# Kernel tuning notes

Hardware: AMD Instinct MI355X
Metric: run time of the kernel (lower is better)

The kernel has to match this reference:

```python
import jax, jax.numpy as jnp
import numpy as np

N_LAYERS = 2
D_CONV = 4
D_MODEL = 768
D_INNER = 1536
D_STATE = 16
D_DELTA = 48
B = 2
L = 1024
EPS = 1e-5


def setup_inputs() -> dict:
    key = jax.random.key(0)
    ks = jax.random.split(key, 8)
    s = 0.02
    x = jax.random.normal(ks[0], (B, L, D_MODEL), jnp.float32)
    in_proj_w = jax.random.normal(ks[1], (N_LAYERS, 2 * D_INNER, D_MODEL), jnp.float32) * s
    conv_w = jax.random.normal(ks[2], (N_LAYERS, D_INNER, 1, D_CONV), jnp.float32) * s
    conv_b = jnp.zeros((N_LAYERS, D_INNER), jnp.float32)
    xproj_w = jax.random.normal(ks[3], (N_LAYERS, D_DELTA + 2 * D_STATE, D_INNER), jnp.float32) * s
    dt_w = jax.random.normal(ks[4], (N_LAYERS, D_INNER, D_DELTA), jnp.float32) * s
    dt_b = jax.random.normal(ks[5], (N_LAYERS, D_INNER), jnp.float32) * s
    A_log = jnp.tile(jnp.log(jnp.arange(1, D_STATE + 1, dtype=jnp.float32)), (N_LAYERS, D_INNER, 1))
    D = jnp.ones((N_LAYERS, D_INNER), jnp.float32)
    out_proj_w = jax.random.normal(ks[6], (N_LAYERS, D_MODEL, D_INNER), jnp.float32) * s
    norm_w = jnp.ones((N_LAYERS, D_MODEL), jnp.float32)
    return dict(x=x, in_proj_w=in_proj_w, conv_w=conv_w, conv_b=conv_b,
                xproj_w=xproj_w, dt_w=dt_w, dt_b=dt_b, A_log=A_log, D=D,
                out_proj_w=out_proj_w, norm_w=norm_w)


def rms_norm(x, w):
    return w * x * jax.lax.rsqrt(jnp.mean(x * x, axis=-1, keepdims=True) + EPS)


def causal_depthwise_conv(x, w, b):
    # x: [B, L, D_INNER], w: [D_INNER, 1, K], b: [D_INNER]
    xc = x.transpose(0, 2, 1)  # [B, D, L]
    y = jax.lax.conv_general_dilated(
        xc, w, window_strides=(1,), padding=[(D_CONV - 1, 0)],
        dimension_numbers=("NCH", "OIH", "NCH"), feature_group_count=D_INNER)
    y = y + b[None, :, None]
    return y.transpose(0, 2, 1)  # [B, L, D]


def ssm(x, A_log, D, xproj_w, dt_w, dt_b):
    # x: [B, L, D_INNER]
    A = -jnp.exp(A_log)  # [D, N]
    dbc = jnp.einsum('bld,ed->ble', x, xproj_w)
    delta, Bc, C = jnp.split(dbc, [D_DELTA, D_DELTA + D_STATE], axis=-1)
    delta = jax.nn.softplus(jnp.einsum('blr,dr->bld', delta, dt_w) + dt_b)  # [B, L, D]
    dA = jnp.exp(delta[..., None] * A)                          # [B, L, D, N]
    dBx = delta[..., None] * Bc[:, :, None, :] * x[..., None]   # [B, L, D, N]

    def step(h, inp):
        dA_t, dBx_t, C_t = inp
        h = dA_t * h + dBx_t                      # [B, D, N]
        y = jnp.einsum('bdn,bn->bd', h, C_t)      # [B, D]
        return h, y

    h0 = jnp.zeros((x.shape[0], D_INNER, D_STATE), x.dtype)
    _, ys = jax.lax.scan(step, h0, (dA.transpose(1, 0, 2, 3),
                                    dBx.transpose(1, 0, 2, 3),
                                    C.transpose(1, 0, 2)))
    y = ys.transpose(1, 0, 2)  # [B, L, D]
    return y + D * x


def mamba_block(x, in_w, cw, cb, xp_w, dtw, dtb, Alog, Dp, out_w):
    xz = jnp.einsum('blm,em->ble', x, in_w)           # [B, L, 2*D_INNER]
    xi, z = jnp.split(xz, 2, axis=-1)
    xi = jax.nn.silu(causal_depthwise_conv(xi, cw, cb))
    y = ssm(xi, Alog, Dp, xp_w, dtw, dtb)
    out = y * jax.nn.silu(z)
    return jnp.einsum('bld,md->blm', out, out_w)


def reference(x, in_proj_w, conv_w, conv_b, xproj_w, dt_w, dt_b, A_log, D, out_proj_w, norm_w):
    for i in range(N_LAYERS):
        x = x + mamba_block(rms_norm(x, norm_w[i]), in_proj_w[i], conv_w[i], conv_b[i],
                            xproj_w[i], dt_w[i], dt_b[i], A_log[i], D[i], out_proj_w[i])
    return x
```

## Files before the change

kernel.cpp:

```cpp
#include <hip/hip_runtime.h>
#include <hip/hip_bf16.h>
#include <cstdint>

#define NL 2
#define DM 768
#define DI 1536
#define DS 16
#define DD 48
#define DCONV 4
#define BB 2
#define LL 1024
#define MROWS (BB*LL)
#define DBCW (DD + 2*DS)
#define TC 16
#define NCH (LL/TC)
#define KSPL 4
#define XPN 128

typedef __bf16 bf16x8 __attribute__((ext_vector_type(8)));
typedef float f32x4 __attribute__((ext_vector_type(4)));
using bf16 = __hip_bfloat16;

__device__ __forceinline__ float softplusf(float x) {
  return (x > 20.f) ? x : log1pf(__expf(x));
}

__device__ __forceinline__ float bfu2f(ushort u) {
  return __uint_as_float((uint32_t)u << 16);
}

__device__ __forceinline__ void load_lds16(const void* g, void* l) {
  __builtin_amdgcn_global_load_lds(
      (const __attribute__((address_space(1))) void*)g,
      (__attribute__((address_space(3))) void*)l, 16, 0, 0);
}

#define WI_N (NL*2*DI*DM)
#define WX_N (NL*XPN*DI)
#define WD_N (NL*DI*DD)
#define WO_N (NL*DM*DI)
__global__ __launch_bounds__(256)
void prep_weights(const float* __restrict__ wi, const float* __restrict__ wx,
                  const float* __restrict__ wd, const float* __restrict__ wo,
                  bf16* __restrict__ bi, bf16* __restrict__ bx,
                  bf16* __restrict__ bd, bf16* __restrict__ bo)
{
  int i = blockIdx.x * 256 + threadIdx.x;
  if (i < WI_N) { bi[i] = __float2bfloat16(wi[i]); return; }
  i -= WI_N;
  if (i < WX_N) {
    const int l = i / (XPN*DI), r = (i / DI) % XPN, k = i % DI;
    const float v = (r < DBCW) ? wx[((size_t)l*DBCW + r)*DI + k] : 0.f;
    bx[i] = __float2bfloat16(v); return;
  }
  i -= WX_N;
  if (i < WD_N) { bd[i] = __float2bfloat16(wd[i]); return; }
  i -= WD_N;
  if (i < WO_N) { bo[i] = __float2bfloat16(wo[i]); }
}

__global__ __launch_bounds__(256)
void rmsnorm_kernel(const float* __restrict__ x, const float* __restrict__ w,
                    bf16* __restrict__ out)
{
  const int row = blockIdx.x;
  const float* xr = x + (size_t)row * DM;
  const int t = threadIdx.x;
  float v0 = xr[t], v1 = xr[t + 256], v2 = xr[t + 512];
  float ss = v0*v0 + v1*v1 + v2*v2;
  #pragma unroll
  for (int off = 32; off > 0; off >>= 1) ss += __shfl_down(ss, off);
  __shared__ float sred[4];
  if ((t & 63) == 0) sred[t >> 6] = ss;
  __syncthreads();
  const float scale = rsqrtf((sred[0]+sred[1]+sred[2]+sred[3]) * (1.f/DM) + 1e-5f);
  out[(size_t)row*DM + t      ] = __float2bfloat16(v0 * scale * w[t]);
  out[(size_t)row*DM + t + 256] = __float2bfloat16(v1 * scale * w[t + 256]);
  out[(size_t)row*DM + t + 512] = __float2bfloat16(v2 * scale * w[t + 512]);
}

__global__ __launch_bounds__(256)
void gemm_in128(const bf16* __restrict__ A, const bf16* __restrict__ W,
                bf16* __restrict__ xb, bf16* __restrict__ zb)
{
  __shared__ __align__(16) bf16 As[128][32];
  __shared__ __align__(16) bf16 Ws[128][32];
  const int tid = threadIdx.x;
  const int wave = tid >> 6, lane = tid & 63;
  const int m0 = blockIdx.x * 128, n0 = blockIdx.y * 128;
  const int wr = (wave >> 1) * 64, wc = (wave & 1) * 64;
  const int l16 = lane & 15, quad = lane >> 4;
  const int srow = wave * 16 + (lane >> 2);
  const int scol = (lane & 3) * 8;
  bf16* a_base0 = &As[wave*16][0];
  bf16* a_base1 = &As[64 + wave*16][0];
  bf16* w_base0 = &Ws[wave*16][0];
  bf16* w_base1 = &Ws[64 + wave*16][0];

  f32x4 acc[4][4] = {};

  for (int k0 = 0; k0 < DM; k0 += 32) {
    load_lds16(A + (size_t)(m0 + srow) * DM + k0 + scol,      a_base0);
    load_lds16(A + (size_t)(m0 + 64 + srow) * DM + k0 + scol, a_base1);
    load_lds16(W + (size_t)(n0 + srow) * DM + k0 + scol,      w_base0);
    load_lds16(W + (size_t)(n0 + 64 + srow) * DM + k0 + scol, w_base1);
    __syncthreads();

    bf16x8 af[4], wf[4];
    #pragma unroll
    for (int i = 0; i < 4; ++i)
      af[i] = *reinterpret_cast<const bf16x8*>(&As[wr + i*16 + l16][quad*8]);
    #pragma unroll
    for (int j = 0; j < 4; ++j)
      wf[j] = *reinterpret_cast<const bf16x8*>(&Ws[wc + j*16 + l16][quad*8]);
    #pragma unroll
    for (int i = 0; i < 4; ++i)
      #pragma unroll
      for (int j = 0; j < 4; ++j)
        acc[i][j] = __builtin_amdgcn_mfma_f32_16x16x32_bf16(af[i], wf[j], acc[i][j], 0, 0, 0);
    __syncthreads();
  }

  const bool isz = (n0 >= DI);
  #pragma unroll
  for (int i = 0; i < 4; ++i) {
    #pragma unroll
    for (int j = 0; j < 4; ++j) {
      const int col = n0 + wc + j*16 + l16;
      #pragma unroll
      for (int r = 0; r < 4; ++r) {
        const int row = m0 + wr + i*16 + quad*4 + r;
        const float v = acc[i][j][r];
        if (!isz) xb[(size_t)row*DI + col]      = __float2bfloat16(v);
        else      zb[(size_t)row*DI + col - DI] = __float2bfloat16(v);
      }
    }
  }
}

template<int MODE>
__global__ __launch_bounds__(256)
void gemm64l(const bf16* __restrict__ A, int lda,
             const bf16* __restrict__ W, int ldw,
             float* __restrict__ C, int ldc, int N, int K,
             const float* __restrict__ res)
{
  __shared__ __align__(16) bf16 As[64][32];
  __shared__ __align__(16) bf16 Ws[64][32];
  const int tid = threadIdx.x;
  const int wave = tid >> 6, lane = tid & 63;
  const int m0 = blockIdx.x * 64, n0 = blockIdx.y * 64;
  const int wr = (wave >> 1) * 32, wc = (wave & 1) * 32;
  const int l16 = lane & 15, quad = lane >> 4;
  const int srow = wave * 16 + (lane >> 2);
  const int scol = (lane & 3) * 8;
  bf16* a_base = &As[wave*16][0];
  bf16* w_base = &Ws[wave*16][0];

  A += (size_t)blockIdx.z * K;
  W += (size_t)blockIdx.z * K;
  C += (size_t)blockIdx.z * MROWS * ldc;

  f32x4 acc[2][2] = {};

  for (int k0 = 0; k0 < K; k0 += 32) {
    load_lds16(A + (size_t)(m0 + srow) * lda + k0 + scol, a_base);
    load_lds16(W + (size_t)(n0 + srow) * ldw + k0 + scol, w_base);
    __syncthreads();
    bf16x8 af[2], wf[2];
    #pragma unroll
    for (int i = 0; i < 2; ++i)
      af[i] = *reinterpret_cast<const bf16x8*>(&As[wr + i*16 + l16][quad*8]);
    #pragma unroll
    for (int j = 0; j < 2; ++j)
      wf[j] = *reinterpret_cast<const bf16x8*>(&Ws[wc + j*16 + l16][quad*8]);
    #pragma unroll
    for (int i = 0; i < 2; ++i)
      #pragma unroll
      for (int j = 0; j < 2; ++j)
        acc[i][j] = __builtin_amdgcn_mfma_f32_16x16x32_bf16(af[i], wf[j], acc[i][j], 0, 0, 0);
    __syncthreads();
  }

  #pragma unroll
  for (int i = 0; i < 2; ++i) {
    #pragma unroll
    for (int j = 0; j < 2; ++j) {
      const int col = n0 + wc + j*16 + l16;
      if (col >= N) continue;
      #pragma unroll
      for (int r = 0; r < 4; ++r) {
        const int row = m0 + wr + i*16 + quad*4 + r;
        float v = acc[i][j][r];
        const size_t idx = (size_t)row * ldc + col;
        if (MODE == 3) v += res[idx];
        C[idx] = v;
      }
    }
  }
}

__global__ __launch_bounds__(256)
void xproj_reduce(const float* __restrict__ part, bf16* __restrict__ dbcb,
                  float* __restrict__ bcf)
{
  const int idx = blockIdx.x * 256 + threadIdx.x;
  const int row = idx / DBCW, col = idx % DBCW;
  float v = part[idx];
  #pragma unroll
  for (int z = 1; z < KSPL; ++z) v += part[idx + (size_t)z*MROWS*DBCW];
  if (col < DD) dbcb[(size_t)row*DD + col] = __float2bfloat16(v);
  else          bcf[(size_t)row*32 + col - DD] = v;
}

__global__ __launch_bounds__(256)
void conv_silu_kernel(const bf16* __restrict__ xb, const float* __restrict__ cw,
                      const float* __restrict__ cb, bf16* __restrict__ xob)
{
  const int idx = blockIdx.x * 256 + threadIdx.x;
  const int d = idx % DI;
  const int row = idx / DI;
  const int l = row % LL;
  float acc = cb[d];
  #pragma unroll
  for (int k = 0; k < DCONV; ++k) {
    const int ll = l - (DCONV-1) + k;
    if (ll >= 0)
      acc += cw[d*DCONV + k] * __bfloat162float(xb[(size_t)(row - (DCONV-1) + k) * DI + d]);
  }
  const float s = acc / (1.f + __expf(-acc));
  xob[idx] = __float2bfloat16(s);
}

__global__ __launch_bounds__(256)
void gemm_dt(const bf16* __restrict__ A, const bf16* __restrict__ W,
             bf16* __restrict__ Cb, const float* __restrict__ bias)
{
  __shared__ __align__(16) bf16 As[64][40];
  __shared__ __align__(16) bf16 Ws[64][40];
  const int tid = threadIdx.x;
  const int m0 = blockIdx.x * 64, n0 = blockIdx.y * 64;
  const int wave = tid >> 6, lane = tid & 63;
  const int wr = (wave >> 1) * 32, wc = (wave & 1) * 32;
  const int l16 = lane & 15, quad = lane >> 4;
  const int srow = tid >> 2;
  const int scol = (tid & 3) * 8;

  f32x4 acc[2][2] = {};

  #pragma unroll
  for (int k0 = 0; k0 < DD; k0 += 32) {
    {
      const bf16* src = A + (size_t)(m0 + srow) * DD + (k0 + scol);
      bf16* dst = &As[srow][scol];
      if (k0 + scol + 8 <= DD) {
        *reinterpret_cast<uint4*>(dst) = *reinterpret_cast<const uint4*>(src);
      } else {
        #pragma unroll
        for (int j = 0; j < 8; ++j)
          dst[j] = (k0 + scol + j < DD) ? src[j] : __float2bfloat16(0.f);
      }
    }
    {
      const bf16* src = W + (size_t)(n0 + srow) * DD + (k0 + scol);
      bf16* dst = &Ws[srow][scol];
      if (k0 + scol + 8 <= DD) {
        *reinterpret_cast<uint4*>(dst) = *reinterpret_cast<const uint4*>(src);
      } else {
        #pragma unroll
        for (int j = 0; j < 8; ++j)
          dst[j] = (k0 + scol + j < DD) ? src[j] : __float2bfloat16(0.f);
      }
    }
    __syncthreads();
    bf16x8 af[2], wf[2];
    #pragma unroll
    for (int i = 0; i < 2; ++i)
      af[i] = *reinterpret_cast<const bf16x8*>(&As[wr + i*16 + l16][quad*8]);
    #pragma unroll
    for (int j = 0; j < 2; ++j)
      wf[j] = *reinterpret_cast<const bf16x8*>(&Ws[wc + j*16 + l16][quad*8]);
    #pragma unroll
    for (int i = 0; i < 2; ++i)
      #pragma unroll
      for (int j = 0; j < 2; ++j)
        acc[i][j] = __builtin_amdgcn_mfma_f32_16x16x32_bf16(af[i], wf[j], acc[i][j], 0, 0, 0);
    __syncthreads();
  }

  #pragma unroll
  for (int i = 0; i < 2; ++i) {
    #pragma unroll
    for (int j = 0; j < 2; ++j) {
      const int col = n0 + wc + j*16 + l16;
      #pragma unroll
      for (int r = 0; r < 4; ++r) {
        const int row = m0 + wr + i*16 + quad*4 + r;
        Cb[(size_t)row*DI + col] = __float2bfloat16(softplusf(acc[i][j][r] + bias[col]));
      }
    }
  }
}

__global__ __launch_bounds__(256)
void scan_pass1(const bf16* __restrict__ delta, const bf16* __restrict__ xi,
                const float* __restrict__ bcf, const float* __restrict__ A_log,
                float* __restrict__ P, float* __restrict__ H)
{
  __shared__ float Bs[TC][DS];
  const int tid = threadIdx.x;
  const int wave = tid >> 6, lane = tid & 63;
  const int s = lane >> 5;
  const int dloc = wave*32 + (lane & 31);
  const int dt = blockIdx.x % (DI/128);
  const int c  = (blockIdx.x / (DI/128)) % NCH;
  const int b  =  blockIdx.x / ((DI/128)*NCH);
  const int d  = dt*128 + dloc;
  const int t0 = c*TC;

  {
    const int t = tid >> 4, n = tid & 15;
    Bs[t][n] = bcf[((size_t)b*LL + t0 + t)*32 + n];
  }

  const ushort* dptr = (const ushort*)(delta + ((size_t)b*LL + t0)*DI + d);
  const ushort* xptr = (const ushort*)(xi    + ((size_t)b*LL + t0)*DI + d);
  ushort dls[TC], xvs[TC];
  #pragma unroll
  for (int t = 0; t < TC; ++t) dls[t] = dptr[(size_t)t*DI];
  #pragma unroll
  for (int t = 0; t < TC; ++t) xvs[t] = xptr[(size_t)t*DI];

  float An[8];
  {
    const float4* ap = (const float4*)(A_log + (size_t)d*DS + s*8);
    float4 v0 = ap[0], v1 = ap[1];
    An[0] = -__expf(v0.x)*1.44269504f; An[1] = -__expf(v0.y)*1.44269504f;
    An[2] = -__expf(v0.z)*1.44269504f; An[3] = -__expf(v0.w)*1.44269504f;
    An[4] = -__expf(v1.x)*1.44269504f; An[5] = -__expf(v1.y)*1.44269504f;
    An[6] = -__expf(v1.z)*1.44269504f; An[7] = -__expf(v1.w)*1.44269504f;
  }
  __syncthreads();

  float h[8] = {0.f,0.f,0.f,0.f,0.f,0.f,0.f,0.f};
  float sdl = 0.f;
  #pragma unroll
  for (int t = 0; t < TC; ++t) {
    const float dl = bfu2f(dls[t]);
    const float xv = bfu2f(xvs[t]);
    const float dlxv = dl * xv;
    sdl += dl;
    const float4* brow = (const float4*)&Bs[t][s*8];
    const float4 b0 = brow[0], b1 = brow[1];
    const float bb[8] = {b0.x,b0.y,b0.z,b0.w,b1.x,b1.y,b1.z,b1.w};
    #pragma unroll
    for (int n = 0; n < 8; ++n) {
      const float dA = exp2f(dl * An[n]);
      h[n] = dA*h[n] + dlxv*bb[n];
    }
  }
  const size_t base = (((size_t)b*NCH + c)*DI + d)*DS + s*8;
  float4* Pp = (float4*)(P + base);
  float4* Hp = (float4*)(H + base);
  Pp[0] = make_float4(exp2f(An[0]*sdl), exp2f(An[1]*sdl), exp2f(An[2]*sdl), exp2f(An[3]*sdl));
  Pp[1] = make_float4(exp2f(An[4]*sdl), exp2f(An[5]*sdl), exp2f(An[6]*sdl), exp2f(An[7]*sdl));
  Hp[0] = make_float4(h[0],h[1],h[2],h[3]);
  Hp[1] = make_float4(h[4],h[5],h[6],h[7]);
}

__global__ __launch_bounds__(256)
void scan_fix(const float* __restrict__ P, float* __restrict__ H)
{
  const int idx = blockIdx.x * 256 + threadIdx.x;
  const int n = idx & 15;
  const int d = (idx >> 4) % DI;
  const int b = idx / (DS * DI);
  float hin = 0.f;
  #pragma unroll 8
  for (int c = 0; c < NCH; ++c) {
    const size_t ic = (((size_t)b*NCH + c)*DI + d)*DS + n;
    const float Pv = P[ic];
    const float Hv = H[ic];
    H[ic] = hin;
    hin = fmaf(Pv, hin, Hv);
  }
}

__global__ __launch_bounds__(256)
void scan_pass2(const bf16* __restrict__ delta, const bf16* __restrict__ xi,
                const float* __restrict__ bcf, const float* __restrict__ A_log,
                const float* __restrict__ H, const float* __restrict__ Dp,
                const bf16* __restrict__ zb, bf16* __restrict__ outb)
{
  __shared__ float Bs[TC][DS];
  __shared__ float Cs[TC][DS];
  const int tid = threadIdx.x;
  const int wave = tid >> 6, lane = tid & 63;
  const int s = lane >> 5;
  const int dloc = wave*32 + (lane & 31);
  const int dt = blockIdx.x % (DI/128);
  const int c  = (blockIdx.x / (DI/128)) % NCH;
  const int b  =  blockIdx.x / ((DI/128)*NCH);
  const int d  = dt*128 + dloc;
  const int t0 = c*TC;

  {
    const int t = tid >> 4, n = tid & 15;
    const size_t r0 = ((size_t)b*LL + t0 + t)*32;
    Bs[t][n] = bcf[r0 + n];
    Cs[t][n] = bcf[r0 + 16 + n];
  }

  const ushort* dptr = (const ushort*)(delta + ((size_t)b*LL + t0)*DI + d);
  const ushort* xptr = (const ushort*)(xi    + ((size_t)b*LL + t0)*DI + d);
  const ushort* zptr = (const ushort*)(zb    + ((size_t)b*LL + t0)*DI + d);
  ushort dls[TC], xvs[TC], zvs[TC];
  #pragma unroll
  for (int t = 0; t < TC; ++t) dls[t] = dptr[(size_t)t*DI];
  #pragma unroll
  for (int t = 0; t < TC; ++t) xvs[t] = xptr[(size_t)t*DI];
  #pragma unroll
  for (int t = 0; t < TC; ++t) zvs[t] = zptr[(size_t)t*DI];

  float An[8];
  {
    const float4* ap = (const float4*)(A_log + (size_t)d*DS + s*8);
    float4 v0 = ap[0], v1 = ap[1];
    An[0] = -__expf(v0.x)*1.44269504f; An[1] = -__expf(v0.y)*1.44269504f;
    An[2] = -__expf(v0.z)*1.44269504f; An[3] = -__expf(v0.w)*1.44269504f;
    An[4] = -__expf(v1.x)*1.44269504f; An[5] = -__expf(v1.y)*1.44269504f;
    An[6] = -__expf(v1.z)*1.44269504f; An[7] = -__expf(v1.w)*1.44269504f;
  }
  const float Dd = Dp[d];
  float h[8];
  {
    const float4* hp = (const float4*)(H + (((size_t)b*NCH + c)*DI + d)*DS + s*8);
    float4 h0 = hp[0], h1 = hp[1];
    h[0]=h0.x; h[1]=h0.y; h[2]=h0.z; h[3]=h0.w;
    h[4]=h1.x; h[5]=h1.y; h[6]=h1.z; h[7]=h1.w;
  }
  __syncthreads();

  bf16* optr = outb + ((size_t)b*LL + t0)*DI + d;

  #pragma unroll
  for (int t = 0; t < TC; ++t) {
    const float dl = bfu2f(dls[t]);
    const float xv = bfu2f(xvs[t]);
    const float zv = bfu2f(zvs[t]);
    const float dlxv = dl * xv;
    const float4* brow = (const float4*)&Bs[t][s*8];
    const float4* crow = (const float4*)&Cs[t][s*8];
    const float4 b0 = brow[0], b1 = brow[1];
    const float4 c0 = crow[0], c1 = crow[1];
    const float bb[8] = {b0.x,b0.y,b0.z,b0.w,b1.x,b1.y,b1.z,b1.w};
    const float cc[8] = {c0.x,c0.y,c0.z,c0.w,c1.x,c1.y,c1.z,c1.w};
    float y = 0.f;
    #pragma unroll
    for (int n = 0; n < 8; ++n) {
      const float dA = exp2f(dl * An[n]);
      h[n] = dA*h[n] + dlxv*bb[n];
      y = fmaf(h[n], cc[n], y);
    }
    y += __shfl_xor(y, 32);
    if (s == 0) {
      const float o = (y + Dd * xv) * (zv / (1.f + __expf(-zv)));
      optr[(size_t)t*DI] = __float2bfloat16(o);
    }
  }
}

extern "C" void kernel_launch(void* const* d_in, const int* in_sizes, int n_in,
                              void* d_out, int out_size, void* d_ws, size_t ws_size,
                              hipStream_t stream)
{
  const float* x_in   = (const float*)d_in[0];
  const float* w_inp  = (const float*)d_in[1];
  const float* w_conv = (const float*)d_in[2];
  const float* b_conv = (const float*)d_in[3];
  const float* w_xprj = (const float*)d_in[4];
  const float* w_dtp  = (const float*)d_in[5];
  const float* b_dt   = (const float*)d_in[6];
  const float* a_log  = (const float*)d_in[7];
  const float* d_par  = (const float*)d_in[8];
  const float* w_outp = (const float*)d_in[9];
  const float* w_norm = (const float*)d_in[10];
  float* xfinal = (float*)d_out;

  char* ws = (char*)d_ws;
  size_t off = 0;
  auto alloc = [&](size_t bytes) -> void* {
    void* p = ws + off;
    off += (bytes + 255) & ~(size_t)255;
    return p;
  };
  bf16*  wb_in  = (bf16*) alloc((size_t)WI_N*2);
  bf16*  wb_xp  = (bf16*) alloc((size_t)WX_N*2);
  bf16*  wb_dt  = (bf16*) alloc((size_t)WD_N*2);
  bf16*  wb_out = (bf16*) alloc((size_t)WO_N*2);
  bf16*  xn     = (bf16*) alloc((size_t)MROWS*DM*2);
  bf16*  xb     = (bf16*) alloc((size_t)MROWS*DI*2);
  bf16*  zb     = (bf16*) alloc((size_t)MROWS*DI*2);
  bf16*  xcb    = (bf16*) alloc((size_t)MROWS*DI*2);
  float* xpart  = (float*)alloc((size_t)KSPL*MROWS*DBCW*4);
  bf16*  dbcb   = (bf16*) alloc((size_t)MROWS*DD*2);
  float* bcf    = (float*)alloc((size_t)MROWS*32*4);
  bf16*  dltb   = (bf16*) alloc((size_t)MROWS*DI*2);
  bf16*  scb    = (bf16*) alloc((size_t)MROWS*DI*2);
  float* x1     = (float*)alloc((size_t)MROWS*DM*4);
  float* Pws    = (float*)alloc((size_t)BB*NCH*DI*DS*4);
  float* Hws    = (float*)alloc((size_t)BB*NCH*DI*DS*4);

  prep_weights<<<(WI_N+WX_N+WD_N+WO_N + 255)/256, 256, 0, stream>>>(
      w_inp, w_xprj, w_dtp, w_outp, wb_in, wb_xp, wb_dt, wb_out);

  const float* xprev = x_in;
  for (int l = 0; l < NL; ++l) {
    rmsnorm_kernel<<<MROWS, 256, 0, stream>>>(xprev, w_norm + l*DM, xn);

    gemm_in128<<<dim3(MROWS/128, (2*DI)/128), 256, 0, stream>>>(
        xn, wb_in + (size_t)l*2*DI*DM, xb, zb);

    conv_silu_kernel<<<(MROWS*DI)/256, 256, 0, stream>>>(
        xb, w_conv + l*DI*DCONV, b_conv + l*DI, xcb);

    gemm64l<0><<<dim3(MROWS/64, XPN/64, KSPL), 256, 0, stream>>>(
        xcb, DI, wb_xp + (size_t)l*XPN*DI, DI, xpart, DBCW, DBCW, DI/KSPL, nullptr);

    xproj_reduce<<<(MROWS*DBCW)/256, 256, 0, stream>>>(xpart, dbcb, bcf);

    gemm_dt<<<dim3(MROWS/64, DI/64), 256, 0, stream>>>(
        dbcb, wb_dt + (size_t)l*DI*DD, dltb, b_dt + l*DI);

    scan_pass1<<<BB*NCH*(DI/128), 256, 0, stream>>>(
        dltb, xcb, bcf, a_log + (size_t)l*DI*DS, Pws, Hws);
    scan_fix<<<(BB*DI*DS)/256, 256, 0, stream>>>(Pws, Hws);
    scan_pass2<<<BB*NCH*(DI/128), 256, 0, stream>>>(
        dltb, xcb, bcf, a_log + (size_t)l*DI*DS, Hws, d_par + l*DI, zb, scb);

    float* xout = (l == NL-1) ? xfinal : x1;
    gemm64l<3><<<dim3(MROWS/64, DM/64, 1), 256, 0, stream>>>(
        scb, DI, wb_out + (size_t)l*DM*DI, DI, xout, DM, DM, DI, xprev);

    xprev = x1;
  }
}
```

Baseline: 364.5 us.

## Fuse x-proj split-K reduce into consumers, vectorize conv, shrink scan carry state

Removes the xproj_reduce kernel: gemm_dt now sums the split-K partials for delta directly while staging its A tile, and both scan passes sum the B/C partials into shared memory themselves. Conv+SiLU processes 8 channels per thread with vector loads and stores. Scan pass1 writes only the per-chunk delta sum instead of full P decay tensors, and scan_fix recomputes the decay with exp2. Scan chunk length doubles to 32. This cuts launches and intermediate traffic at the cost of redundant partial reductions and higher register pressure in the scan kernels.

Result: no change. 364.5 us (+0.0%).

```diff
diff --git a/kernel.cpp b/kernel.cpp
--- a/kernel.cpp
+++ b/kernel.cpp
@@ -12,13 +12,14 @@
 #define LL 1024
 #define MROWS (BB*LL)
 #define DBCW (DD + 2*DS)
-#define TC 16
+#define TC 32
 #define NCH (LL/TC)
 #define KSPL 4
 #define XPN 128
 
 typedef __bf16 bf16x8 __attribute__((ext_vector_type(8)));
 typedef float f32x4 __attribute__((ext_vector_type(4)));
+typedef ushort ushort8 __attribute__((ext_vector_type(8)));
 using bf16 = __hip_bfloat16;
 
 __device__ __forceinline__ float softplusf(float x) {
@@ -27,6 +28,11 @@
 
 __device__ __forceinline__ float bfu2f(ushort u) {
   return __uint_as_float((uint32_t)u << 16);
+}
+
+__device__ __forceinline__ ushort f2bfu(float f) {
+  const bf16 h = __float2bfloat16(f);
+  return *reinterpret_cast<const ushort*>(&h);
 }
 
 __device__ __forceinline__ void load_lds16(const void* g, void* l) {
@@ -201,39 +207,51 @@
 }
 
 __global__ __launch_bounds__(256)
-void xproj_reduce(const float* __restrict__ part, bf16* __restrict__ dbcb,
-                  float* __restrict__ bcf)
-{
-  const int idx = blockIdx.x * 256 + threadIdx.x;
-  const int row = idx / DBCW, col = idx % DBCW;
-  float v = part[idx];
-  #pragma unroll
-  for (int z = 1; z < KSPL; ++z) v += part[idx + (size_t)z*MROWS*DBCW];
-  if (col < DD) dbcb[(size_t)row*DD + col] = __float2bfloat16(v);
-  else          bcf[(size_t)row*32 + col - DD] = v;
-}
-
-__global__ __launch_bounds__(256)
 void conv_silu_kernel(const bf16* __restrict__ xb, const float* __restrict__ cw,
                       const float* __restrict__ cb, bf16* __restrict__ xob)
 {
   const int idx = blockIdx.x * 256 + threadIdx.x;
-  const int d = idx % DI;
-  const int row = idx / DI;
+  const int d8 = idx % (DI/8);
+  const int row = idx / (DI/8);
   const int l = row % LL;
-  float acc = cb[d];
+  const int d0 = d8 * 8;
+
+  float4 cwv[8];
+  #pragma unroll
+  for (int j = 0; j < 8; ++j)
+    cwv[j] = reinterpret_cast<const float4*>(cw)[d0 + j];
+
+  float acc[8];
+  {
+    const float4* cbp = reinterpret_cast<const float4*>(cb + d0);
+    float4 c0 = cbp[0], c1 = cbp[1];
+    acc[0]=c0.x; acc[1]=c0.y; acc[2]=c0.z; acc[3]=c0.w;
+    acc[4]=c1.x; acc[5]=c1.y; acc[6]=c1.z; acc[7]=c1.w;
+  }
   #pragma unroll
   for (int k = 0; k < DCONV; ++k) {
     const int ll = l - (DCONV-1) + k;
-    if (ll >= 0)
-      acc += cw[d*DCONV + k] * __bfloat162float(xb[(size_t)(row - (DCONV-1) + k) * DI + d]);
-  }
-  const float s = acc / (1.f + __expf(-acc));
-  xob[idx] = __float2bfloat16(s);
-}
-
-__global__ __launch_bounds__(256)
-void gemm_dt(const bf16* __restrict__ A, const bf16* __restrict__ W,
+    if (ll >= 0) {
+      const ushort8 v = *reinterpret_cast<const ushort8*>(
+          xb + (size_t)(row - (DCONV-1) + k) * DI + d0);
+      #pragma unroll
+      for (int j = 0; j < 8; ++j) {
+        const float w = (k==0) ? cwv[j].x : (k==1) ? cwv[j].y : (k==2) ? cwv[j].z : cwv[j].w;
+        acc[j] += w * bfu2f(v[j]);
+      }
+    }
+  }
+  ushort8 o;
+  #pragma unroll
+  for (int j = 0; j < 8; ++j) {
+    const float s = acc[j] / (1.f + __expf(-acc[j]));
+    o[j] = f2bfu(s);
+  }
+  *reinterpret_cast<ushort8*>(xob + (size_t)row*DI + d0) = o;
+}
+
+__global__ __launch_bounds__(256)
+void gemm_dt(const float* __restrict__ xpart, const bf16* __restrict__ W,
              bf16* __restrict__ Cb, const float* __restrict__ bias)
 {
   __shared__ __align__(16) bf16 As[64][40];
@@ -251,14 +269,22 @@
   #pragma unroll
   for (int k0 = 0; k0 < DD; k0 += 32) {
     {
-      const bf16* src = A + (size_t)(m0 + srow) * DD + (k0 + scol);
+      const int cbase = k0 + scol;
       bf16* dst = &As[srow][scol];
-      if (k0 + scol + 8 <= DD) {
-        *reinterpret_cast<uint4*>(dst) = *reinterpret_cast<const uint4*>(src);
+      if (cbase < DD) {
+        float a[8] = {0,0,0,0,0,0,0,0};
+        #pragma unroll
+        for (int z = 0; z < KSPL; ++z) {
+          const float4* p = reinterpret_cast<const float4*>(
+              xpart + (size_t)z*MROWS*DBCW + (size_t)(m0 + srow)*DBCW + cbase);
+          const float4 u = p[0], v = p[1];
+          a[0]+=u.x; a[1]+=u.y; a[2]+=u.z; a[3]+=u.w;
+          a[4]+=v.x; a[5]+=v.y; a[6]+=v.z; a[7]+=v.w;
+        }
+        #pragma unroll
+        for (int j = 0; j < 8; ++j) dst[j] = __float2bfloat16(a[j]);
       } else {
-        #pragma unroll
-        for (int j = 0; j < 8; ++j)
-          dst[j] = (k0 + scol + j < DD) ? src[j] : __float2bfloat16(0.f);
+        *reinterpret_cast<uint4*>(dst) = make_uint4(0,0,0,0);
       }
     }
     {
@@ -304,8 +330,8 @@
 
 __global__ __launch_bounds__(256)
 void scan_pass1(const bf16* __restrict__ delta, const bf16* __restrict__ xi,
-                const float* __restrict__ bcf, const float* __restrict__ A_log,
-                float* __restrict__ P, float* __restrict__ H)
+                const float* __restrict__ xpart, const float* __restrict__ A_log,
+                float* __restrict__ sdl_out, float* __restrict__ H)
 {
   __shared__ float Bs[TC][DS];
   const int tid = threadIdx.x;
@@ -318,9 +344,13 @@
   const int d  = dt*128 + dloc;
   const int t0 = c*TC;
 
-  {
-    const int t = tid >> 4, n = tid & 15;
-    Bs[t][n] = bcf[((size_t)b*LL + t0 + t)*32 + n];
+  for (int i = tid; i < TC*DS; i += 256) {
+    const int t = i >> 4, n = i & 15;
+    const size_t rb = ((size_t)b*LL + t0 + t)*DBCW + DD + n;
+    float v = xpart[rb];
+    #pragma unroll
+    for (int z = 1; z < KSPL; ++z) v += xpart[rb + (size_t)z*(MROWS*DBCW)];
+    Bs[t][n] = v;
   }
 
   const ushort* dptr = (const ushort*)(delta + ((size_t)b*LL + t0)*DI + d);
@@ -343,13 +373,13 @@
   __syncthreads();
 
   float h[8] = {0.f,0.f,0.f,0.f,0.f,0.f,0.f,0.f};
-  float sdl = 0.f;
+  float sacc = 0.f;
   #pragma unroll
   for (int t = 0; t < TC; ++t) {
     const float dl = bfu2f(dls[t]);
     const float xv = bfu2f(xvs[t]);
     const float dlxv = dl * xv;
-    sdl += dl;
+    sacc += dl;
     const float4* brow = (const float4*)&Bs[t][s*8];
     const float4 b0 = brow[0], b1 = brow[1];
     const float bb[8] = {b0.x,b0.y,b0.z,b0.w,b1.x,b1.y,b1.z,b1.w};
@@ -360,26 +390,26 @@
     }
   }
   const size_t base = (((size_t)b*NCH + c)*DI + d)*DS + s*8;
-  float4* Pp = (float4*)(P + base);
   float4* Hp = (float4*)(H + base);
-  Pp[0] = make_float4(exp2f(An[0]*sdl), exp2f(An[1]*sdl), exp2f(An[2]*sdl), exp2f(An[3]*sdl));
-  Pp[1] = make_float4(exp2f(An[4]*sdl), exp2f(An[5]*sdl), exp2f(An[6]*sdl), exp2f(An[7]*sdl));
   Hp[0] = make_float4(h[0],h[1],h[2],h[3]);
   Hp[1] = make_float4(h[4],h[5],h[6],h[7]);
-}
-
-__global__ __launch_bounds__(256)
-void scan_fix(const float* __restrict__ P, float* __restrict__ H)
+  if (s == 0) sdl_out[((size_t)b*NCH + c)*DI + d] = sacc;
+}
+
+__global__ __launch_bounds__(256)
+void scan_fix(const float* __restrict__ sdl, const float* __restrict__ A_log,
+              float* __restrict__ H)
 {
   const int idx = blockIdx.x * 256 + threadIdx.x;
   const int n = idx & 15;
   const int d = (idx >> 4) % DI;
   const int b = idx / (DS * DI);
+  const float An = -__expf(A_log[(size_t)d*DS + n]) * 1.44269504f;
   float hin = 0.f;
   #pragma unroll 8
   for (int c = 0; c < NCH; ++c) {
+    const float Pv = exp2f(An * sdl[((size_t)b*NCH + c)*DI + d]);
     const size_t ic = (((size_t)b*NCH + c)*DI + d)*DS + n;
-    const float Pv = P[ic];
     const float Hv = H[ic];
     H[ic] = hin;
     hin = fmaf(Pv, hin, Hv);
@@ -388,7 +418,7 @@
 
 __global__ __launch_bounds__(256)
 void scan_pass2(const bf16* __restrict__ delta, const bf16* __restrict__ xi,
-                const float* __restrict__ bcf, const float* __restrict__ A_log,
+                const float* __restrict__ xpart, const float* __restrict__ A_log,
                 const float* __restrict__ H, const float* __restrict__ Dp,
                 const bf16* __restrict__ zb, bf16* __restrict__ outb)
 {
@@ -404,11 +434,14 @@
   const int d  = dt*128 + dloc;
   const int t0 = c*TC;
 
-  {
-    const int t = tid >> 4, n = tid & 15;
-    const size_t r0 = ((size_t)b*LL + t0 + t)*32;
-    Bs[t][n] = bcf[r0 + n];
-    Cs[t][n] = bcf[r0 + 16 + n];
+  for (int i = tid; i < TC*2*DS; i += 256) {
+    const int t = i >> 5, n32 = i & 31;
+    const size_t rb = ((size_t)b*LL + t0 + t)*DBCW + DD + n32;
+    float v = xpart[rb];
+    #pragma unroll
+    for (int z = 1; z < KSPL; ++z) v += xpart[rb + (size_t)z*(MROWS*DBCW)];
+    if (n32 < DS) Bs[t][n32] = v;
+    else          Cs[t][n32 - DS] = v;
   }
 
   const ushort* dptr = (const ushort*)(delta + ((size_t)b*LL + t0)*DI + d);
@@ -503,12 +536,10 @@
   bf16*  zb     = (bf16*) alloc((size_t)MROWS*DI*2);
   bf16*  xcb    = (bf16*) alloc((size_t)MROWS*DI*2);
   float* xpart  = (float*)alloc((size_t)KSPL*MROWS*DBCW*4);
-  bf16*  dbcb   = (bf16*) alloc((size_t)MROWS*DD*2);
-  float* bcf    = (float*)alloc((size_t)MROWS*32*4);
   bf16*  dltb   = (bf16*) alloc((size_t)MROWS*DI*2);
   bf16*  scb    = (bf16*) alloc((size_t)MROWS*DI*2);
   float* x1     = (float*)alloc((size_t)MROWS*DM*4);
-  float* Pws    = (float*)alloc((size_t)BB*NCH*DI*DS*4);
+  float* sdlw   = (float*)alloc((size_t)BB*NCH*DI*4);
   float* Hws    = (float*)alloc((size_t)BB*NCH*DI*DS*4);
 
   prep_weights<<<(WI_N+WX_N+WD_N+WO_N + 255)/256, 256, 0, stream>>>(
@@ -521,22 +552,21 @@
     gemm_in128<<<dim3(MROWS/128, (2*DI)/128), 256, 0, stream>>>(
         xn, wb_in + (size_t)l*2*DI*DM, xb, zb);
 
-    conv_silu_kernel<<<(MROWS*DI)/256, 256, 0, stream>>>(
+    conv_silu_kernel<<<(MROWS*DI/8)/256, 256, 0, stream>>>(
         xb, w_conv + l*DI*DCONV, b_conv + l*DI, xcb);
 
     gemm64l<0><<<dim3(MROWS/64, XPN/64, KSPL), 256, 0, stream>>>(
         xcb, DI, wb_xp + (size_t)l*XPN*DI, DI, xpart, DBCW, DBCW, DI/KSPL, nullptr);
 
-    xproj_reduce<<<(MROWS*DBCW)/256, 256, 0, stream>>>(xpart, dbcb, bcf);
-
     gemm_dt<<<dim3(MROWS/64, DI/64), 256, 0, stream>>>(
-        dbcb, wb_dt + (size_t)l*DI*DD, dltb, b_dt + l*DI);
+        xpart, wb_dt + (size_t)l*DI*DD, dltb, b_dt + l*DI);
 
     scan_pass1<<<BB*NCH*(DI/128), 256, 0, stream>>>(
-        dltb, xcb, bcf, a_log + (size_t)l*DI*DS, Pws, Hws);
-    scan_fix<<<(BB*DI*DS)/256, 256, 0, stream>>>(Pws, Hws);
+        dltb, xcb, xpart, a_log + (size_t)l*DI*DS, sdlw, Hws);
+    scan_fix<<<(BB*DI*DS)/256, 256, 0, stream>>>(
+        sdlw, a_log + (size_t)l*DI*DS, Hws);
     scan_pass2<<<BB*NCH*(DI/128), 256, 0, stream>>>(
-        dltb, xcb, bcf, a_log + (size_t)l*DI*DS, Hws, d_par + l*DI, zb, scb);
+        dltb, xcb, xpart, a_log + (size_t)l*DI*DS, Hws, d_par + l*DI, zb, scb);
 
     float* xout = (l == NL-1) ? xfinal : x1;
     gemm64l<3><<<dim3(MROWS/64, DM/64, 1), 256, 0, stream>>>(
```
